# Optimization experiments

Measured on AMD Instinct MI355X. Metric: run time of the kernel, lower is better.

## Reference

```python
import jax, jax.numpy as jnp
import numpy as np

B, H, N, D, RPE = 2, 8, 4096, 64, 64
LAYERS = 3


def _rms(x):
    # SimpleRMSNorm: x / sqrt(mean(x^2) + eps), no learned scale
    return x / jnp.sqrt(jnp.mean(x * x, axis=-1, keepdims=True) + 1e-8)


def setup_inputs() -> dict:
    key = jax.random.key(0)
    ks = jax.random.split(key, 7)
    s = 1.0 / np.sqrt(RPE)
    return {
        "x": jax.random.normal(ks[0], (B, H, N, D), dtype=jnp.float32),
        "w_in": jax.random.normal(ks[1], (1, RPE), dtype=jnp.float32) * 0.5,
        "b_in": jax.random.normal(ks[2], (RPE,), dtype=jnp.float32) * 0.02,
        "w_hid": jax.random.normal(ks[3], (LAYERS, RPE, RPE), dtype=jnp.float32) * s,
        "b_hid": jax.random.normal(ks[4], (LAYERS, RPE), dtype=jnp.float32) * 0.02,
        "w_out": jax.random.normal(ks[5], (RPE, H * D), dtype=jnp.float32) * s,
        "b_out": jax.random.normal(ks[6], (H * D,), dtype=jnp.float32) * 0.02,
    }


def reference(x, w_in, b_in, w_hid, b_hid, w_out, b_out):
    n = x.shape[-2]
    dt = x.dtype

    def rpe(idx):  # idx: (m, 1) relative-position features
        h = idx @ w_in + b_in  # (m, RPE)
        for i in range(LAYERS):  # non-residual: x = layer(x)
            h = jax.nn.relu(_rms(h)) @ w_hid[i] + b_hid[i]
        h = jax.nn.relu(_rms(h)) @ w_out + b_out  # (m, H*D)
        return h.reshape(-1, H, D).transpose(1, 0, 2)  # (H, m, D)

    zero_idx = jnp.ones((1, 1), dt)
    pos_idx = (1.0 / jnp.arange(2, n + 1, dtype=dt)).reshape(n - 1, 1)
    neg_idx = (-1.0 / jnp.arange(n, 1, -1, dtype=dt)).reshape(n - 1, 1)

    zero_k = rpe(zero_idx)  # (H, 1, D); used for both T[0] slots like the torch code
    a = jnp.concatenate([zero_k, rpe(pos_idx), zero_k, rpe(neg_idx)], axis=1)  # (H, 2n, D)
    # act_type='none' -> identity activation on a

    # Toeplitz matvec as circular conv of length 2n via FFT
    y = jnp.fft.rfft(x, 2 * n, axis=-2)          # (B, H, n+1, D) complex
    v = jnp.fft.rfft(a, 2 * n, axis=-2)[None]    # (1, H, n+1, D) complex
    out = jnp.fft.irfft(v * y, 2 * n, axis=-2)[:, :, :n, :]
    return out.astype(dt)
```

## Files before the change

### kernel.cpp

```cpp
#include <hip/hip_runtime.h>

#define N_SEQ 4096
#define N_FFT 8192
#define LAYERS 3
#define FT 512
#define PIDX(i) ((i) + ((i) >> 5))

template<int M>
__device__ inline void pass16_fwd(float* re, float* im, int tid)
{
    const int Q = M >> 4;
    const int j = tid & (Q - 1);
    const int G = tid / Q;
    const int base = G * M + j;
    const float KR[4] = {1.f, 0.9238795325f, 0.7071067812f, 0.3826834324f};
    const float KI[4] = {0.f, -0.3826834324f, -0.7071067812f, -0.9238795325f};
    float xr[4][4], xi[4][4];
#pragma unroll
    for (int a = 0; a < 4; ++a)
#pragma unroll
        for (int b = 0; b < 4; ++b) {
            int idx = PIDX(base + a * (M >> 2) + b * Q);
            xr[a][b] = re[idx]; xi[a][b] = im[idx];
        }
    float cj, sj;
    __sincosf(-6.283185307179586f / (float)M * (float)j, &sj, &cj);
#pragma unroll
    for (int b = 0; b < 4; ++b) {
        float c1 = cj * KR[b] - sj * KI[b];
        float s1 = cj * KI[b] + sj * KR[b];
        float c2 = c1 * c1 - s1 * s1, s2 = 2.f * c1 * s1;
        float c3 = c2 * c1 - s2 * s1, s3 = c2 * s1 + s2 * c1;
        float ar = xr[0][b] + xr[2][b], ai = xi[0][b] + xi[2][b];
        float br = xr[0][b] - xr[2][b], bi = xi[0][b] - xi[2][b];
        float cr = xr[1][b] + xr[3][b], ci = xi[1][b] + xi[3][b];
        float dr = xi[1][b] - xi[3][b], di = -(xr[1][b] - xr[3][b]);
        xr[0][b] = ar + cr;               xi[0][b] = ai + ci;
        float t1r = br + dr, t1i = bi + di;
        xr[1][b] = t1r * c1 - t1i * s1;   xi[1][b] = t1r * s1 + t1i * c1;
        float t2r = ar - cr, t2i = ai - ci;
        xr[2][b] = t2r * c2 - t2i * s2;   xi[2][b] = t2r * s2 + t2i * c2;
        float t3r = br - dr, t3i = bi - di;
        xr[3][b] = t3r * c3 - t3i * s3;   xi[3][b] = t3r * s3 + t3i * c3;
    }
    {
        float e1c = cj * cj - sj * sj, e1s = 2.f * cj * sj;
        float c1 = e1c * e1c - e1s * e1s, s1 = 2.f * e1c * e1s;
        float c2 = c1 * c1 - s1 * s1, s2 = 2.f * c1 * s1;
        float c3 = c2 * c1 - s2 * s1, s3 = c2 * s1 + s2 * c1;
#pragma unroll
        for (int a = 0; a < 4; ++a) {
            float ar = xr[a][0] + xr[a][2], ai = xi[a][0] + xi[a][2];
            float br = xr[a][0] - xr[a][2], bi = xi[a][0] - xi[a][2];
            float cr = xr[a][1] + xr[a][3], ci = xi[a][1] + xi[a][3];
            float dr = xi[a][1] - xi[a][3], di = -(xr[a][1] - xr[a][3]);
            xr[a][0] = ar + cr;               xi[a][0] = ai + ci;
            float t1r = br + dr, t1i = bi + di;
            xr[a][1] = t1r * c1 - t1i * s1;   xi[a][1] = t1r * s1 + t1i * c1;
            float t2r = ar - cr, t2i = ai - ci;
            xr[a][2] = t2r * c2 - t2i * s2;   xi[a][2] = t2r * s2 + t2i * c2;
            float t3r = br - dr, t3i = bi - di;
            xr[a][3] = t3r * c3 - t3i * s3;   xi[a][3] = t3r * s3 + t3i * c3;
        }
    }
#pragma unroll
    for (int a = 0; a < 4; ++a)
#pragma unroll
        for (int b = 0; b < 4; ++b) {
            int idx = PIDX(base + a * (M >> 2) + b * Q);
            re[idx] = xr[a][b]; im[idx] = xi[a][b];
        }
}

template<int M>
__device__ inline void pass16_inv(float* re, float* im, int tid)
{
    const int Q = M >> 4;
    const int j = tid & (Q - 1);
    const int G = tid / Q;
    const int base = G * M + j;
    const float KR[4] = {1.f, 0.9238795325f, 0.7071067812f, 0.3826834324f};
    const float KI[4] = {0.f, 0.3826834324f, 0.7071067812f, 0.9238795325f};
    float xr[4][4], xi[4][4];
#pragma unroll
    for (int a = 0; a < 4; ++a)
#pragma unroll
        for (int b = 0; b < 4; ++b) {
            int idx = PIDX(base + a * (M >> 2) + b * Q);
            xr[a][b] = re[idx]; xi[a][b] = im[idx];
        }
    float cj, sj;
    __sincosf(6.283185307179586f / (float)M * (float)j, &sj, &cj);
    {
        float e1c = cj * cj - sj * sj, e1s = 2.f * cj * sj;
        float c1 = e1c * e1c - e1s * e1s, s1 = 2.f * e1c * e1s;
        float c2 = c1 * c1 - s1 * s1, s2 = 2.f * c1 * s1;
        float c3 = c2 * c1 - s2 * s1, s3 = c2 * s1 + s2 * c1;
#pragma unroll
        for (int a = 0; a < 4; ++a) {
            float t0r = xr[a][0], t0i = xi[a][0];
            float t1r = xr[a][1] * c1 - xi[a][1] * s1, t1i = xr[a][1] * s1 + xi[a][1] * c1;
            float t2r = xr[a][2] * c2 - xi[a][2] * s2, t2i = xr[a][2] * s2 + xi[a][2] * c2;
            float t3r = xr[a][3] * c3 - xi[a][3] * s3, t3i = xr[a][3] * s3 + xi[a][3] * c3;
            float pr = t0r + t2r, pi = t0i + t2i;
            float qr = t0r - t2r, qi = t0i - t2i;
            float rr = t1r + t3r, ri = t1i + t3i;
            float sr = -(t1i - t3i), si = t1r - t3r;
            xr[a][0] = pr + rr; xi[a][0] = pi + ri;
            xr[a][1] = qr + sr; xi[a][1] = qi + si;
            xr[a][2] = pr - rr; xi[a][2] = pi - ri;
            xr[a][3] = qr - sr; xi[a][3] = qi - si;
        }
    }
#pragma unroll
    for (int b = 0; b < 4; ++b) {
        float c1 = cj * KR[b] - sj * KI[b];
        float s1 = cj * KI[b] + sj * KR[b];
        float c2 = c1 * c1 - s1 * s1, s2 = 2.f * c1 * s1;
        float c3 = c2 * c1 - s2 * s1, s3 = c2 * s1 + s2 * c1;
        float t0r = xr[0][b], t0i = xi[0][b];
        float t1r = xr[1][b] * c1 - xi[1][b] * s1, t1i = xr[1][b] * s1 + xi[1][b] * c1;
        float t2r = xr[2][b] * c2 - xi[2][b] * s2, t2i = xr[2][b] * s2 + xi[2][b] * c2;
        float t3r = xr[3][b] * c3 - xi[3][b] * s3, t3i = xr[3][b] * s3 + xi[3][b] * c3;
        float pr = t0r + t2r, pi = t0i + t2i;
        float qr = t0r - t2r, qi = t0i - t2i;
        float rr = t1r + t3r, ri = t1i + t3i;
        float sr = -(t1i - t3i), si = t1r - t3r;
        xr[0][b] = pr + rr; xi[0][b] = pi + ri;
        xr[1][b] = qr + sr; xi[1][b] = qi + si;
        xr[2][b] = pr - rr; xi[2][b] = pi - ri;
        xr[3][b] = qr - sr; xi[3][b] = qi - si;
    }
#pragma unroll
    for (int a = 0; a < 4; ++a)
#pragma unroll
        for (int b = 0; b < 4; ++b) {
            int idx = PIDX(base + a * (M >> 2) + b * Q);
            re[idx] = xr[a][b]; im[idx] = xi[a][b];
        }
}

__device__ inline void fwd8(float* zr, float* zi, int o)
{
    const float R = 0.70710678118654752f;
    {
        float ar = zr[o] + zr[o+4], ai = zi[o] + zi[o+4];
        float br = zr[o] - zr[o+4], bi = zi[o] - zi[o+4];
        float cr = zr[o+2] + zr[o+6], ci = zi[o+2] + zi[o+6];
        float dr = zi[o+2] - zi[o+6], di = -(zr[o+2] - zr[o+6]);
        zr[o]   = ar + cr; zi[o]   = ai + ci;
        zr[o+2] = br + dr; zi[o+2] = bi + di;
        zr[o+4] = ar - cr; zi[o+4] = ai - ci;
        zr[o+6] = br - dr; zi[o+6] = bi - di;
    }
    {
        float ar = zr[o+1] + zr[o+5], ai = zi[o+1] + zi[o+5];
        float br = zr[o+1] - zr[o+5], bi = zi[o+1] - zi[o+5];
        float cr = zr[o+3] + zr[o+7], ci = zi[o+3] + zi[o+7];
        float dr = zi[o+3] - zi[o+7], di = -(zr[o+3] - zr[o+7]);
        zr[o+1] = ar + cr; zi[o+1] = ai + ci;
        float t1r = br + dr, t1i = bi + di;
        zr[o+3] = R * (t1r + t1i); zi[o+3] = R * (t1i - t1r);
        float t2r = ar - cr, t2i = ai - ci;
        zr[o+5] = t2i;  zi[o+5] = -t2r;
        float t3r = br - dr, t3i = bi - di;
        zr[o+7] = R * (t3i - t3r); zi[o+7] = -R * (t3r + t3i);
    }
#pragma unroll
    for (int p = 0; p < 8; p += 2) {
        float ur = zr[o+p], ui = zi[o+p], vr = zr[o+p+1], vi = zi[o+p+1];
        zr[o+p]   = ur + vr; zi[o+p]   = ui + vi;
        zr[o+p+1] = ur - vr; zi[o+p+1] = ui - vi;
    }
}

__device__ inline void inv8(float* zr, float* zi, int o)
{
    const float R = 0.70710678118654752f;
#pragma unroll
    for (int p = 0; p < 8; p += 2) {
        float ur = zr[o+p], ui = zi[o+p], vr = zr[o+p+1], vi = zi[o+p+1];
        zr[o+p]   = ur + vr; zi[o+p]   = ui + vi;
        zr[o+p+1] = ur - vr; zi[o+p+1] = ui - vi;
    }
    {
        float t0r = zr[o],   t0i = zi[o];
        float t1r = zr[o+2], t1i = zi[o+2];
        float t2r = zr[o+4], t2i = zi[o+4];
        float t3r = zr[o+6], t3i = zi[o+6];
        float pr = t0r + t2r, pi = t0i + t2i;
        float qr = t0r - t2r, qi = t0i - t2i;
        float rr = t1r + t3r, ri = t1i + t3i;
        float sr = -(t1i - t3i), si = t1r - t3r;
        zr[o]   = pr + rr; zi[o]   = pi + ri;
        zr[o+2] = qr + sr; zi[o+2] = qi + si;
        zr[o+4] = pr - rr; zi[o+4] = pi - ri;
        zr[o+6] = qr - sr; zi[o+6] = qi - si;
    }
    {
        float t0r = zr[o+1], t0i = zi[o+1];
        float yr = zr[o+3], yi = zi[o+3];
        float t1r = R * (yr - yi), t1i = R * (yr + yi);
        yr = zr[o+5]; yi = zi[o+5];
        float t2r = -yi, t2i = yr;
        yr = zr[o+7]; yi = zi[o+7];
        float t3r = -R * (yr + yi), t3i = R * (yr - yi);
        float pr = t0r + t2r, pi = t0i + t2i;
        float qr = t0r - t2r, qi = t0i - t2i;
        float rr = t1r + t3r, ri = t1i + t3i;
        float sr = -(t1i - t3i), si = t1r - t3r;
        zr[o+1] = pr + rr; zi[o+1] = pi + ri;
        zr[o+3] = qr + sr; zi[o+3] = qi + si;
        zr[o+5] = pr - rr; zi[o+5] = pi - ri;
        zr[o+7] = qr - sr; zi[o+7] = qi - si;
    }
}

__global__ __launch_bounds__(512, 4) void prep_kernel(
    const float* __restrict__ x,
    const float* __restrict__ w_in, const float* __restrict__ b_in,
    const float* __restrict__ w_hid, const float* __restrict__ b_hid,
    const float* __restrict__ w_out, const float* __restrict__ b_out,
    float* __restrict__ a_t, float2* __restrict__ xt2)
{
    __shared__ __align__(16) char smem[43264];
    const int tid = threadIdx.x;

    if (blockIdx.x >= 256) {
        float (*t0)[65] = (float (*)[65])smem;
        float (*t1)[65] = (float (*)[65])(smem + 16640);
        int bb = blockIdx.x - 256;
        int h = bb >> 6;
        int nb = bb & 63;
        int lx = tid & 63;
        int ly = tid >> 6;
        const float* s0 = x + ((size_t)h * N_SEQ + nb * 64) * 64;
        const float* s1 = x + ((size_t)(8 + h) * N_SEQ + nb * 64) * 64;
        for (int r = ly; r < 64; r += 8) {
            t0[r][lx] = s0[r * 64 + lx];
            t1[r][lx] = s1[r * 64 + lx];
        }
        __syncthreads();
        for (int r = ly; r < 64; r += 8) {
            float2* dst = xt2 + (size_t)(h * 64 + r) * N_SEQ + nb * 64;
            dst[lx] = make_float2(t0[lx][r], t1[lx][r]);
        }
        return;
    }

    float (*ubuf)[65] = (float (*)[65])smem;
    float (*sums)[17] = (float (*)[17])(smem + 8320);
    float4* wl        = (float4*)(smem + 10496);

    {
        const int p = tid & 31;
        const int s = tid >> 5;
        const int pos = blockIdx.x * 32 + p;
        float v;
        if (pos == 0 || pos == N_SEQ) v = 1.0f;
        else if (pos < N_SEQ)         v = 1.0f / (float)(pos + 1);
        else                          v = -1.0f / (float)(2 * N_SEQ + 1 - pos);

        float h[4];
#pragma unroll
        for (int i = 0; i < 4; ++i) {
            int f = s * 4 + i;
            h[i] = v * w_in[f] + b_in[f];
        }
        for (int L = 0; L < LAYERS; ++L) {
            const float4* wsrc = (const float4*)(w_hid + L * 4096);
            wl[tid] = wsrc[tid];
            wl[tid + 512] = wsrc[tid + 512];
            float s2 = h[0]*h[0] + h[1]*h[1] + h[2]*h[2] + h[3]*h[3];
            sums[p][s] = s2;
            __syncthreads();
            float tot = 0.f;
#pragma unroll
            for (int g = 0; g < 16; ++g) tot += sums[p][g];
            float r = rsqrtf(tot * (1.f / 64.f) + 1e-8f);
#pragma unroll
            for (int i = 0; i < 4; ++i)
                ubuf[p][s * 4 + i] = fmaxf(h[i] * r, 0.f);
            __syncthreads();
            float acc[4];
#pragma unroll
            for (int i = 0; i < 4; ++i) acc[i] = b_hid[L * 64 + s * 4 + i];
#pragma unroll 8
            for (int j = 0; j < 64; ++j) {
                float uj = ubuf[p][j];
                float4 w = wl[j * 16 + s];
                acc[0] = fmaf(uj, w.x, acc[0]); acc[1] = fmaf(uj, w.y, acc[1]);
                acc[2] = fmaf(uj, w.z, acc[2]); acc[3] = fmaf(uj, w.w, acc[3]);
            }
#pragma unroll
            for (int i = 0; i < 4; ++i) h[i] = acc[i];
            __syncthreads();
        }
        float s2 = h[0]*h[0] + h[1]*h[1] + h[2]*h[2] + h[3]*h[3];
        sums[p][s] = s2;
        __syncthreads();
        float tot = 0.f;
#pragma unroll
        for (int g = 0; g < 16; ++g) tot += sums[p][g];
        float r = rsqrtf(tot * (1.f / 64.f) + 1e-8f);
#pragma unroll
        for (int i = 0; i < 4; ++i)
            ubuf[p][s * 4 + i] = fmaxf(h[i] * r, 0.f);
        __syncthreads();
    }

    {
        const int o  = tid >> 3;
        const int pg = tid & 7;
        const int pos0 = blockIdx.x * 32;
        float4* wt = wl;
        float acc[8][4];
#pragma unroll
        for (int ii = 0; ii < 8; ++ii) {
            float bo = b_out[o * 8 + ii];
#pragma unroll
            for (int i = 0; i < 4; ++i) acc[ii][i] = bo;
        }
        for (int jc = 0; jc < 4; ++jc) {
            float4 wreg[4];
#pragma unroll
            for (int k = 0; k < 4; ++k) {
                int i4 = k * 512 + tid;
                int jj = i4 >> 7, f4 = i4 & 127;
                wreg[k] = *(const float4*)(w_out + (jc * 16 + jj) * 512 + f4 * 4);
            }
            __syncthreads();
#pragma unroll
            for (int k = 0; k < 4; ++k) {
                int i4 = k * 512 + tid;
                wt[i4] = wreg[k];
            }
            __syncthreads();
#pragma unroll
            for (int jj = 0; jj < 16; ++jj) {
                int j = jc * 16 + jj;
                float4 w0 = wt[jj * 128 + o * 2];
                float4 w1 = wt[jj * 128 + o * 2 + 1];
                float u0 = ubuf[pg * 4 + 0][j];
                float u1 = ubuf[pg * 4 + 1][j];
                float u2 = ubuf[pg * 4 + 2][j];
                float u3 = ubuf[pg * 4 + 3][j];
                acc[0][0] = fmaf(u0, w0.x, acc[0][0]); acc[0][1] = fmaf(u1, w0.x, acc[0][1]);
                acc[0][2] = fmaf(u2, w0.x, acc[0][2]); acc[0][3] = fmaf(u3, w0.x, acc[0][3]);
                acc[1][0] = fmaf(u0, w0.y, acc[1][0]); acc[1][1] = fmaf(u1, w0.y, acc[1][1]);
                acc[1][2] = fmaf(u2, w0.y, acc[1][2]); acc[1][3] = fmaf(u3, w0.y, acc[1][3]);
                acc[2][0] = fmaf(u0, w0.z, acc[2][0]); acc[2][1] = fmaf(u1, w0.z, acc[2][1]);
                acc[2][2] = fmaf(u2, w0.z, acc[2][2]); acc[2][3] = fmaf(u3, w0.z, acc[2][3]);
                acc[3][0] = fmaf(u0, w0.w, acc[3][0]); acc[3][1] = fmaf(u1, w0.w, acc[3][1]);
                acc[3][2] = fmaf(u2, w0.w, acc[3][2]); acc[3][3] = fmaf(u3, w0.w, acc[3][3]);
                acc[4][0] = fmaf(u0, w1.x, acc[4][0]); acc[4][1] = fmaf(u1, w1.x, acc[4][1]);
                acc[4][2] = fmaf(u2, w1.x, acc[4][2]); acc[4][3] = fmaf(u3, w1.x, acc[4][3]);
                acc[5][0] = fmaf(u0, w1.y, acc[5][0]); acc[5][1] = fmaf(u1, w1.y, acc[5][1]);
                acc[5][2] = fmaf(u2, w1.y, acc[5][2]); acc[5][3] = fmaf(u3, w1.y, acc[5][3]);
                acc[6][0] = fmaf(u0, w1.z, acc[6][0]); acc[6][1] = fmaf(u1, w1.z, acc[6][1]);
                acc[6][2] = fmaf(u2, w1.z, acc[6][2]); acc[6][3] = fmaf(u3, w1.z, acc[6][3]);
                acc[7][0] = fmaf(u0, w1.w, acc[7][0]); acc[7][1] = fmaf(u1, w1.w, acc[7][1]);
                acc[7][2] = fmaf(u2, w1.w, acc[7][2]); acc[7][3] = fmaf(u3, w1.w, acc[7][3]);
            }
            __syncthreads();
        }
#pragma unroll
        for (int ii = 0; ii < 8; ++ii) {
            int f = o * 8 + ii;
#pragma unroll
            for (int i = 0; i < 4; ++i)
                a_t[(size_t)f * N_FFT + pos0 + pg * 4 + i] = acc[ii][i];
        }
    }
}

__global__ __launch_bounds__(FT, 2) void conv_kernel(const float* __restrict__ a_t,
                                                     const float2* __restrict__ xt2,
                                                     float2* __restrict__ out_t2)
{
    __shared__ float re[8448];
    __shared__ float im[8448];
    const int tid = threadIdx.x;
    const int hd = blockIdx.x;
    const float JR = 0.9238795325f;
    const float JI = -0.3826834324f;

    {
        const float* src = a_t + (size_t)hd * N_FFT;
        float ck, sk;
        __sincosf(-6.283185307179586f / 8192.f * (float)tid, &sk, &ck);
#pragma unroll
        for (int pp = 0; pp < 4; ++pp) {
            int k = pp * FT + tid;
            float x0 = src[k], x1 = src[k + 2048], x2 = src[k + 4096], x3 = src[k + 6144];
            float ar = x0 + x2, br = x0 - x2;
            float cr = x1 + x3, e = x1 - x3;
            re[PIDX(k)] = ar + cr; im[PIDX(k)] = 0.f;
            float c1 = ck, s1 = sk;
            float c2 = c1 * c1 - s1 * s1, s2 = 2.f * c1 * s1;
            float c3 = c2 * c1 - s2 * s1, s3 = c2 * s1 + s2 * c1;
            re[PIDX(k + 2048)] = br * c1 + e * s1;  im[PIDX(k + 2048)] = br * s1 - e * c1;
            float t2r = ar - cr;
            re[PIDX(k + 4096)] = t2r * c2;          im[PIDX(k + 4096)] = t2r * s2;
            re[PIDX(k + 6144)] = br * c3 - e * s3;  im[PIDX(k + 6144)] = br * s3 + e * c3;
            float tc = ck * JR - sk * JI; sk = ck * JI + sk * JR; ck = tc;
        }
    }
    __syncthreads();
    pass16_fwd<2048>(re, im, tid);
    __syncthreads();
    pass16_fwd<128>(re, im, tid);
    __syncthreads();
    float afr[16], afi[16];
    {
        const int base = tid * 16;
#pragma unroll
        for (int c = 0; c < 16; ++c) { int idx = PIDX(base + c); afr[c] = re[idx]; afi[c] = im[idx]; }
        fwd8(afr, afi, 0); fwd8(afr, afi, 8);
    }
    __syncthreads();
    {
        const float2* src = xt2 + (size_t)hd * N_SEQ;
        float ck, sk;
        __sincosf(-6.283185307179586f / 8192.f * (float)tid, &sk, &ck);
#pragma unroll
        for (int pp = 0; pp < 4; ++pp) {
            int k = pp * FT + tid;
            float2 z0 = src[k], z1 = src[k + 2048];
            float ar = z0.x, ai = z0.y;
            float cr = z1.x, ci = z1.y;
            float dr = z1.y, di = -z1.x;
            re[PIDX(k)] = ar + cr; im[PIDX(k)] = ai + ci;
            float c1 = ck, s1 = sk;
            float c2 = c1 * c1 - s1 * s1, s2 = 2.f * c1 * s1;
            float c3 = c2 * c1 - s2 * s1, s3 = c2 * s1 + s2 * c1;
            float t1r = ar + dr, t1i = ai + di;
            re[PIDX(k + 2048)] = t1r * c1 - t1i * s1; im[PIDX(k + 2048)] = t1r * s1 + t1i * c1;
            float t2r = ar - cr, t2i = ai - ci;
            re[PIDX(k + 4096)] = t2r * c2 - t2i * s2; im[PIDX(k + 4096)] = t2r * s2 + t2i * c2;
            float t3r = ar - dr, t3i = ai - di;
            re[PIDX(k + 6144)] = t3r * c3 - t3i * s3; im[PIDX(k + 6144)] = t3r * s3 + t3i * c3;
            float tc = ck * JR - sk * JI; sk = ck * JI + sk * JR; ck = tc;
        }
    }
    __syncthreads();
    pass16_fwd<2048>(re, im, tid);
    __syncthreads();
    pass16_fwd<128>(re, im, tid);
    __syncthreads();
    {
        const int base = tid * 16;
        float zr[16], zi[16];
#pragma unroll
        for (int c = 0; c < 16; ++c) { int idx = PIDX(base + c); zr[c] = re[idx]; zi[c] = im[idx]; }
        fwd8(zr, zi, 0); fwd8(zr, zi, 8);
        const float inv = 1.0f / (float)N_FFT;
#pragma unroll
        for (int c = 0; c < 16; ++c) {
            float xr = zr[c], xi_ = zi[c];
            zr[c] = (xr * afr[c] - xi_ * afi[c]) * inv;
            zi[c] = (xr * afi[c] + xi_ * afr[c]) * inv;
        }
        inv8(zr, zi, 0); inv8(zr, zi, 8);
#pragma unroll
        for (int c = 0; c < 16; ++c) { int idx = PIDX(base + c); re[idx] = zr[c]; im[idx] = zi[c]; }
    }
    __syncthreads();
    pass16_inv<128>(re, im, tid);
    __syncthreads();
    pass16_inv<2048>(re, im, tid);
    __syncthreads();
    {
        float2* dst = out_t2 + (size_t)hd * N_SEQ;
        float ck, sk;
        __sincosf(6.283185307179586f / 8192.f * (float)tid, &sk, &ck);
        const float JcR = 0.9238795325f, JcI = 0.3826834324f;
#pragma unroll
        for (int pp = 0; pp < 4; ++pp) {
            int k = pp * FT + tid;
            float c1 = ck, s1 = sk;
            float c2 = c1 * c1 - s1 * s1, s2 = 2.f * c1 * s1;
            float c3 = c2 * c1 - s2 * s1, s3 = c2 * s1 + s2 * c1;
            float t0r = re[PIDX(k)],        t0i = im[PIDX(k)];
            float y1r = re[PIDX(k + 2048)], y1i = im[PIDX(k + 2048)];
            float y2r = re[PIDX(k + 4096)], y2i = im[PIDX(k + 4096)];
            float y3r = re[PIDX(k + 6144)], y3i = im[PIDX(k + 6144)];
            float t1r = y1r * c1 - y1i * s1, t1i = y1r * s1 + y1i * c1;
            float t2r = y2r * c2 - y2i * s2, t2i = y2r * s2 + y2i * c2;
            float t3r = y3r * c3 - y3i * s3, t3i = y3r * s3 + y3i * c3;
            float pr = t0r + t2r, pi = t0i + t2i;
            float qr = t0r - t2r, qi = t0i - t2i;
            float rr = t1r + t3r, ri = t1i + t3i;
            float sr = -(t1i - t3i), si = t1r - t3r;
            dst[k]        = make_float2(pr + rr, pi + ri);
            dst[k + 2048] = make_float2(qr + sr, qi + si);
            float tc = ck * JcR - sk * JcI; sk = ck * JcI + sk * JcR; ck = tc;
        }
    }
}

__global__ __launch_bounds__(256) void transpose_o_kernel(const float2* __restrict__ out_t2,
                                                          float* __restrict__ out)
{
    __shared__ float t0[64][65];
    __shared__ float t1[64][65];
    int h = blockIdx.x >> 6;
    int nb = blockIdx.x & 63;
    int lx = threadIdx.x & 63;
    int ly = threadIdx.x >> 6;
    for (int r = ly; r < 64; r += 4) {
        float2 v = out_t2[(size_t)(h * 64 + r) * N_SEQ + nb * 64 + lx];
        t0[r][lx] = v.x;
        t1[r][lx] = v.y;
    }
    __syncthreads();
    float* d0 = out + ((size_t)h * N_SEQ + nb * 64) * 64;
    float* d1 = out + ((size_t)(8 + h) * N_SEQ + nb * 64) * 64;
    for (int r = ly; r < 64; r += 4) {
        d0[r * 64 + lx] = t0[lx][r];
        d1[r * 64 + lx] = t1[lx][r];
    }
}

extern "C" void kernel_launch(void* const* d_in, const int* in_sizes, int n_in,
                              void* d_out, int out_size, void* d_ws, size_t ws_size,
                              hipStream_t stream)
{
    const float* x     = (const float*)d_in[0];
    const float* w_in  = (const float*)d_in[1];
    const float* b_in  = (const float*)d_in[2];
    const float* w_hid = (const float*)d_in[3];
    const float* b_hid = (const float*)d_in[4];
    const float* w_out = (const float*)d_in[5];
    const float* b_out = (const float*)d_in[6];
    float* out = (float*)d_out;

    char* ws = (char*)d_ws;
    float2* xt2    = (float2*)ws;
    float*  a_t    = (float*)(ws + (size_t)16 * 1024 * 1024);
    float2* out_t2 = (float2*)(ws + (size_t)32 * 1024 * 1024);

    prep_kernel<<<768, 512, 0, stream>>>(x, w_in, b_in, w_hid, b_hid, w_out, b_out,
                                         a_t, xt2);
    conv_kernel<<<512, FT, 0, stream>>>(a_t, xt2, out_t2);
    transpose_o_kernel<<<512, 256, 0, stream>>>(out_t2, out);
}
```

Before: 143.3 us.

## Restructure FFT conv as radix-8 head plus per-wave 1024-point sub-FFTs

Reworks the 8192-point FFT convolution kernel. A radix-8 first stage now runs in registers on global loads and stores, and the remaining 1024-point sub-transforms are each owned by a single wavefront. This lets the middle passes use wave-level barriers instead of block-wide __syncthreads. Shared memory moves from split re/im arrays to interleaved float2 with vectorized float4 accesses and new padding, and occupancy is raised to 4 blocks. The aim is to cut barrier overhead and LDS traffic. The cost is a more complex index layout, plus higher shared-memory use per block that may limit the requested occupancy.

```diff
diff --git a/kernel.cpp b/kernel.cpp
--- a/kernel.cpp
+++ b/kernel.cpp
@@ -4,15 +4,140 @@
 #define N_FFT 8192
 #define LAYERS 3
 #define FT 512
-#define PIDX(i) ((i) + ((i) >> 5))
+
+#define IDX2(i) ((i) + (((i) >> 5) << 1))
+
+#define WSYNC() { asm volatile("s_waitcnt lgkmcnt(0)" ::: "memory"); __builtin_amdgcn_wave_barrier(); }
+
+__device__ __forceinline__ float2 cmulf(float2 a, float2 b) {
+    return make_float2(fmaf(a.x, b.x, -a.y * b.y), fmaf(a.x, b.y, a.y * b.x));
+}
+__device__ __forceinline__ float2 cmulcf(float2 a, float2 b) {
+    return make_float2(fmaf(a.x, b.x, a.y * b.y), fmaf(a.y, b.x, -a.x * b.y));
+}
+__device__ __forceinline__ float2 f2a(float2 a, float2 b) { return make_float2(a.x + b.x, a.y + b.y); }
+__device__ __forceinline__ float2 f2s(float2 a, float2 b) { return make_float2(a.x - b.x, a.y - b.y); }
+
+__device__ __forceinline__ void twchain(int np, float2* T)
+{
+    float c1, s1;
+    __sincosf(-7.6699039394282061e-4f * (float)np, &s1, &c1);
+    T[1] = make_float2(c1, s1);
+    T[2] = cmulf(T[1], T[1]);
+    T[3] = cmulf(T[2], T[1]);
+    T[4] = cmulf(T[2], T[2]);
+    T[5] = cmulf(T[3], T[2]);
+    T[6] = cmulf(T[3], T[3]);
+    T[7] = cmulf(T[4], T[3]);
+}
+
+__device__ __forceinline__ void ahead8(const float* x, int np, float2* X)
+{
+    const float R2 = 0.70710678118654752f;
+    float p0 = x[0] + x[4], q0 = x[0] - x[4];
+    float p1 = x[2] + x[6], q1 = x[2] - x[6];
+    float r0 = x[1] + x[5], t0 = x[1] - x[5];
+    float r1 = x[3] + x[7], t1 = x[3] - x[7];
+    float e0 = p0 + p1, e2 = p0 - p1;
+    float o0 = r0 + r1, o2 = r0 - r1;
+    float rm = R2 * (t0 - t1), rp = R2 * (t0 + t1);
+    X[0] = make_float2(e0 + o0, 0.f);
+    X[4] = make_float2(e0 - o0, 0.f);
+    X[2] = make_float2(e2, -o2);
+    X[6] = make_float2(e2,  o2);
+    X[1] = make_float2(q0 + rm, -q1 - rp);
+    X[5] = make_float2(q0 - rm, -q1 + rp);
+    X[3] = make_float2(q0 - rm,  q1 - rp);
+    X[7] = make_float2(q0 + rm,  q1 + rp);
+    float2 T[8];
+    twchain(np, T);
+#pragma unroll
+    for (int q = 1; q < 8; ++q) X[q] = cmulf(X[q], T[q]);
+}
+
+__device__ __forceinline__ void zhead8(const float2* z, int np, float2* X)
+{
+    const float R2 = 0.70710678118654752f;
+    float2 A0 = f2a(z[0], z[2]);
+    float2 A2 = f2s(z[0], z[2]);
+    float2 A1 = make_float2(z[0].x + z[2].y, z[0].y - z[2].x);
+    float2 A3 = make_float2(z[0].x - z[2].y, z[0].y + z[2].x);
+    float2 B0 = f2a(z[1], z[3]);
+    float2 bm = f2s(z[1], z[3]);
+    float2 B2 = make_float2(bm.y, -bm.x);
+    float2 u1 = make_float2(z[1].x + z[3].y, z[1].y - z[3].x);
+    float2 B1 = make_float2(R2 * (u1.x + u1.y), R2 * (u1.y - u1.x));
+    float2 u3 = make_float2(z[1].x - z[3].y, z[1].y + z[3].x);
+    float2 B3 = make_float2(R2 * (u3.y - u3.x), -R2 * (u3.x + u3.y));
+    X[0] = f2a(A0, B0); X[4] = f2s(A0, B0);
+    X[1] = f2a(A1, B1); X[5] = f2s(A1, B1);
+    X[2] = f2a(A2, B2); X[6] = f2s(A2, B2);
+    X[3] = f2a(A3, B3); X[7] = f2s(A3, B3);
+    float2 T[8];
+    twchain(np, T);
+#pragma unroll
+    for (int q = 1; q < 8; ++q) X[q] = cmulf(X[q], T[q]);
+}
+
+__device__ __forceinline__ void ihead8(const float2* v, int np, float2* u)
+{
+    const float R2 = 0.70710678118654752f;
+    float2 T[8];
+    twchain(np, T);
+    float2 V[8];
+    V[0] = v[0];
+#pragma unroll
+    for (int q = 1; q < 8; ++q) V[q] = cmulcf(v[q], T[q]);
+    float2 s0 = f2a(V[0], V[4]), d0 = f2s(V[0], V[4]);
+    float2 s1 = f2a(V[1], V[5]), d1 = f2s(V[1], V[5]);
+    float2 s2 = f2a(V[2], V[6]), d2 = f2s(V[2], V[6]);
+    float2 s3 = f2a(V[3], V[7]), d3 = f2s(V[3], V[7]);
+    u[0] = f2a(f2a(s0, s1), f2a(s2, s3));
+    u[2] = make_float2((s0.x - s2.x) - (s1.y - s3.y),
+                       (s0.y - s2.y) + (s1.x - s3.x));
+    float m1 = R2 * (d1.x - d1.y), p1 = R2 * (d1.x + d1.y);
+    float m3 = R2 * (d3.x - d3.y), p3 = R2 * (d3.x + d3.y);
+    u[1] = make_float2(d0.x + m1 - d2.y - p3, d0.y + p1 + d2.x + m3);
+    u[3] = make_float2(d0.x - p1 + d2.y + m3, d0.y + m1 - d2.x + p3);
+}
+
+__device__ __forceinline__ void tail4_fwd(float2* y)
+{
+#pragma unroll
+    for (int g = 0; g < 16; g += 4) {
+        float2 a = f2a(y[g],     y[g + 2]);
+        float2 b = f2s(y[g],     y[g + 2]);
+        float2 c = f2a(y[g + 1], y[g + 3]);
+        float2 w = f2s(y[g + 1], y[g + 3]);
+        float2 d = make_float2(w.y, -w.x);
+        y[g]     = f2a(a, c);
+        y[g + 1] = f2a(b, d);
+        y[g + 2] = f2s(a, c);
+        y[g + 3] = f2s(b, d);
+    }
+}
+__device__ __forceinline__ void tail4_inv(float2* y)
+{
+#pragma unroll
+    for (int g = 0; g < 16; g += 4) {
+        float2 a = f2a(y[g],     y[g + 2]);
+        float2 b = f2s(y[g],     y[g + 2]);
+        float2 c = f2a(y[g + 1], y[g + 3]);
+        float2 d = f2s(y[g + 1], y[g + 3]);
+        float2 id = make_float2(-d.y, d.x);
+        y[g]     = f2a(a, c);
+        y[g + 2] = f2s(a, c);
+        y[g + 1] = f2a(b, id);
+        y[g + 3] = f2s(b, id);
+    }
+}
 
 template<int M>
-__device__ inline void pass16_fwd(float* re, float* im, int tid)
+__device__ __forceinline__ void wpass16_fwd(float2* buf, int C, int lane)
 {
     const int Q = M >> 4;
-    const int j = tid & (Q - 1);
-    const int G = tid / Q;
-    const int base = G * M + j;
+    const int j = lane & (Q - 1);
+    const int base = C + (lane / Q) * M + j;
     const float KR[4] = {1.f, 0.9238795325f, 0.7071067812f, 0.3826834324f};
     const float KI[4] = {0.f, -0.3826834324f, -0.7071067812f, -0.9238795325f};
     float xr[4][4], xi[4][4];
@@ -20,8 +145,8 @@
     for (int a = 0; a < 4; ++a)
 #pragma unroll
         for (int b = 0; b < 4; ++b) {
-            int idx = PIDX(base + a * (M >> 2) + b * Q);
-            xr[a][b] = re[idx]; xi[a][b] = im[idx];
+            float2 v = buf[IDX2(base + a * (M >> 2) + b * Q)];
+            xr[a][b] = v.x; xi[a][b] = v.y;
         }
     float cj, sj;
     __sincosf(-6.283185307179586f / (float)M * (float)j, &sj, &cj);
@@ -66,19 +191,16 @@
 #pragma unroll
     for (int a = 0; a < 4; ++a)
 #pragma unroll
-        for (int b = 0; b < 4; ++b) {
-            int idx = PIDX(base + a * (M >> 2) + b * Q);
-            re[idx] = xr[a][b]; im[idx] = xi[a][b];
-        }
+        for (int b = 0; b < 4; ++b)
+            buf[IDX2(base + a * (M >> 2) + b * Q)] = make_float2(xr[a][b], xi[a][b]);
 }
 
 template<int M>
-__device__ inline void pass16_inv(float* re, float* im, int tid)
+__device__ __forceinline__ void wpass16_inv(float2* buf, int C, int lane)
 {
     const int Q = M >> 4;
-    const int j = tid & (Q - 1);
-    const int G = tid / Q;
-    const int base = G * M + j;
+    const int j = lane & (Q - 1);
+    const int base = C + (lane / Q) * M + j;
     const float KR[4] = {1.f, 0.9238795325f, 0.7071067812f, 0.3826834324f};
     const float KI[4] = {0.f, 0.3826834324f, 0.7071067812f, 0.9238795325f};
     float xr[4][4], xi[4][4];
@@ -86,8 +208,8 @@
     for (int a = 0; a < 4; ++a)
 #pragma unroll
         for (int b = 0; b < 4; ++b) {
-            int idx = PIDX(base + a * (M >> 2) + b * Q);
-            xr[a][b] = re[idx]; xi[a][b] = im[idx];
+            float2 v = buf[IDX2(base + a * (M >> 2) + b * Q)];
+            xr[a][b] = v.x; xi[a][b] = v.y;
         }
     float cj, sj;
     __sincosf(6.283185307179586f / (float)M * (float)j, &sj, &cj);
@@ -134,86 +256,8 @@
 #pragma unroll
     for (int a = 0; a < 4; ++a)
 #pragma unroll
-        for (int b = 0; b < 4; ++b) {
-            int idx = PIDX(base + a * (M >> 2) + b * Q);
-            re[idx] = xr[a][b]; im[idx] = xi[a][b];
-        }
-}
-
-__device__ inline void fwd8(float* zr, float* zi, int o)
-{
-    const float R = 0.70710678118654752f;
-    {
-        float ar = zr[o] + zr[o+4], ai = zi[o] + zi[o+4];
-        float br = zr[o] - zr[o+4], bi = zi[o] - zi[o+4];
-        float cr = zr[o+2] + zr[o+6], ci = zi[o+2] + zi[o+6];
-        float dr = zi[o+2] - zi[o+6], di = -(zr[o+2] - zr[o+6]);
-        zr[o]   = ar + cr; zi[o]   = ai + ci;
-        zr[o+2] = br + dr; zi[o+2] = bi + di;
-        zr[o+4] = ar - cr; zi[o+4] = ai - ci;
-        zr[o+6] = br - dr; zi[o+6] = bi - di;
-    }
-    {
-        float ar = zr[o+1] + zr[o+5], ai = zi[o+1] + zi[o+5];
-        float br = zr[o+1] - zr[o+5], bi = zi[o+1] - zi[o+5];
-        float cr = zr[o+3] + zr[o+7], ci = zi[o+3] + zi[o+7];
-        float dr = zi[o+3] - zi[o+7], di = -(zr[o+3] - zr[o+7]);
-        zr[o+1] = ar + cr; zi[o+1] = ai + ci;
-        float t1r = br + dr, t1i = bi + di;
-        zr[o+3] = R * (t1r + t1i); zi[o+3] = R * (t1i - t1r);
-        float t2r = ar - cr, t2i = ai - ci;
-        zr[o+5] = t2i;  zi[o+5] = -t2r;
-        float t3r = br - dr, t3i = bi - di;
-        zr[o+7] = R * (t3i - t3r); zi[o+7] = -R * (t3r + t3i);
-    }
-#pragma unroll
-    for (int p = 0; p < 8; p += 2) {
-        float ur = zr[o+p], ui = zi[o+p], vr = zr[o+p+1], vi = zi[o+p+1];
-        zr[o+p]   = ur + vr; zi[o+p]   = ui + vi;
-        zr[o+p+1] = ur - vr; zi[o+p+1] = ui - vi;
-    }
-}
-
-__device__ inline void inv8(float* zr, float* zi, int o)
-{
-    const float R = 0.70710678118654752f;
-#pragma unroll
-    for (int p = 0; p < 8; p += 2) {
-        float ur = zr[o+p], ui = zi[o+p], vr = zr[o+p+1], vi = zi[o+p+1];
-        zr[o+p]   = ur + vr; zi[o+p]   = ui + vi;
-        zr[o+p+1] = ur - vr; zi[o+p+1] = ui - vi;
-    }
-    {
-        float t0r = zr[o],   t0i = zi[o];
-        float t1r = zr[o+2], t1i = zi[o+2];
-        float t2r = zr[o+4], t2i = zi[o+4];
-        float t3r = zr[o+6], t3i = zi[o+6];
-        float pr = t0r + t2r, pi = t0i + t2i;
-        float qr = t0r - t2r, qi = t0i - t2i;
-        float rr = t1r + t3r, ri = t1i + t3i;
-        float sr = -(t1i - t3i), si = t1r - t3r;
-        zr[o]   = pr + rr; zi[o]   = pi + ri;
-        zr[o+2] = qr + sr; zi[o+2] = qi + si;
-        zr[o+4] = pr - rr; zi[o+4] = pi - ri;
-        zr[o+6] = qr - sr; zi[o+6] = qi - si;
-    }
-    {
-        float t0r = zr[o+1], t0i = zi[o+1];
-        float yr = zr[o+3], yi = zi[o+3];
-        float t1r = R * (yr - yi), t1i = R * (yr + yi);
-        yr = zr[o+5]; yi = zi[o+5];
-        float t2r = -yi, t2i = yr;
-        yr = zr[o+7]; yi = zi[o+7];
-        float t3r = -R * (yr + yi), t3i = R * (yr - yi);
-        float pr = t0r + t2r, pi = t0i + t2i;
-        float qr = t0r - t2r, qi = t0i - t2i;
-        float rr = t1r + t3r, ri = t1i + t3i;
-        float sr = -(t1i - t3i), si = t1r - t3r;
-        zr[o+1] = pr + rr; zi[o+1] = pi + ri;
-        zr[o+3] = qr + sr; zi[o+3] = qi + si;
-        zr[o+5] = pr - rr; zi[o+5] = pi - ri;
-        zr[o+7] = qr - sr; zi[o+7] = qi - si;
-    }
+        for (int b = 0; b < 4; ++b)
+            buf[IDX2(base + a * (M >> 2) + b * Q)] = make_float2(xr[a][b], xi[a][b]);
 }
 
 __global__ __launch_bounds__(512, 4) void prep_kernel(
@@ -374,128 +418,113 @@
     }
 }
 
-__global__ __launch_bounds__(FT, 2) void conv_kernel(const float* __restrict__ a_t,
+__global__ __launch_bounds__(FT, 4) void conv_kernel(const float* __restrict__ a_t,
                                                      const float2* __restrict__ xt2,
                                                      float2* __restrict__ out_t2)
 {
-    __shared__ float re[8448];
-    __shared__ float im[8448];
+    __shared__ __align__(16) float2 buf[8704];
     const int tid = threadIdx.x;
+    const int lane = tid & 63;
+    const int C = (tid >> 6) << 10;
     const int hd = blockIdx.x;
-    const float JR = 0.9238795325f;
-    const float JI = -0.3826834324f;
-
-    {
-        const float* src = a_t + (size_t)hd * N_FFT;
-        float ck, sk;
-        __sincosf(-6.283185307179586f / 8192.f * (float)tid, &sk, &ck);
-#pragma unroll
-        for (int pp = 0; pp < 4; ++pp) {
-            int k = pp * FT + tid;
-            float x0 = src[k], x1 = src[k + 2048], x2 = src[k + 4096], x3 = src[k + 6144];
-            float ar = x0 + x2, br = x0 - x2;
-            float cr = x1 + x3, e = x1 - x3;
-            re[PIDX(k)] = ar + cr; im[PIDX(k)] = 0.f;
-            float c1 = ck, s1 = sk;
-            float c2 = c1 * c1 - s1 * s1, s2 = 2.f * c1 * s1;
-            float c3 = c2 * c1 - s2 * s1, s3 = c2 * s1 + s2 * c1;
-            re[PIDX(k + 2048)] = br * c1 + e * s1;  im[PIDX(k + 2048)] = br * s1 - e * c1;
-            float t2r = ar - cr;
-            re[PIDX(k + 4096)] = t2r * c2;          im[PIDX(k + 4096)] = t2r * s2;
-            re[PIDX(k + 6144)] = br * c3 - e * s3;  im[PIDX(k + 6144)] = br * s3 + e * c3;
-            float tc = ck * JR - sk * JI; sk = ck * JI + sk * JR; ck = tc;
-        }
+
+    {
+        const float2* asrc = (const float2*)(a_t + (size_t)hd * N_FFT);
+        float2 av[8];
+#pragma unroll
+        for (int p = 0; p < 8; ++p) av[p] = asrc[tid + 512 * p];
+        float xa[8], xb[8];
+#pragma unroll
+        for (int p = 0; p < 8; ++p) { xa[p] = av[p].x; xb[p] = av[p].y; }
+        float2 X0[8], X1[8];
+        ahead8(xa, 2 * tid,     X0);
+        ahead8(xb, 2 * tid + 1, X1);
+#pragma unroll
+        for (int q = 0; q < 8; ++q)
+            *(float4*)&buf[IDX2(q * 1024 + 2 * tid)] =
+                make_float4(X0[q].x, X0[q].y, X1[q].x, X1[q].y);
     }
     __syncthreads();
-    pass16_fwd<2048>(re, im, tid);
+    wpass16_fwd<1024>(buf, C, lane);
+    WSYNC();
+    wpass16_fwd<64>(buf, C, lane);
+    WSYNC();
+    float2 asp[16];
+#pragma unroll
+    for (int k = 0; k < 8; ++k) {
+        float4 v = *(const float4*)&buf[IDX2(C + 16 * lane + 2 * k)];
+        asp[2 * k]     = make_float2(v.x, v.y);
+        asp[2 * k + 1] = make_float2(v.z, v.w);
+    }
+    tail4_fwd(asp);
+    float4 zl[4];
+    {
+        const float4* zsrc = (const float4*)(xt2 + (size_t)hd * N_SEQ);
+#pragma unroll
+        for (int p = 0; p < 4; ++p) zl[p] = zsrc[tid + 512 * p];
+    }
     __syncthreads();
-    pass16_fwd<128>(re, im, tid);
+    {
+        float2 z0[4], z1[4];
+#pragma unroll
+        for (int p = 0; p < 4; ++p) {
+            z0[p] = make_float2(zl[p].x, zl[p].y);
+            z1[p] = make_float2(zl[p].z, zl[p].w);
+        }
+        float2 X0[8], X1[8];
+        zhead8(z0, 2 * tid,     X0);
+        zhead8(z1, 2 * tid + 1, X1);
+#pragma unroll
+        for (int q = 0; q < 8; ++q)
+            *(float4*)&buf[IDX2(q * 1024 + 2 * tid)] =
+                make_float4(X0[q].x, X0[q].y, X1[q].x, X1[q].y);
+    }
     __syncthreads();
-    float afr[16], afi[16];
-    {
-        const int base = tid * 16;
-#pragma unroll
-        for (int c = 0; c < 16; ++c) { int idx = PIDX(base + c); afr[c] = re[idx]; afi[c] = im[idx]; }
-        fwd8(afr, afi, 0); fwd8(afr, afi, 8);
-    }
+    wpass16_fwd<1024>(buf, C, lane);
+    WSYNC();
+    wpass16_fwd<64>(buf, C, lane);
+    WSYNC();
+    {
+        float2 zp[16];
+#pragma unroll
+        for (int k = 0; k < 8; ++k) {
+            float4 v = *(const float4*)&buf[IDX2(C + 16 * lane + 2 * k)];
+            zp[2 * k]     = make_float2(v.x, v.y);
+            zp[2 * k + 1] = make_float2(v.z, v.w);
+        }
+        tail4_fwd(zp);
+        const float inv = 1.0f / (float)N_FFT;
+#pragma unroll
+        for (int c = 0; c < 16; ++c) {
+            float2 m = cmulf(zp[c], asp[c]);
+            zp[c] = make_float2(m.x * inv, m.y * inv);
+        }
+        tail4_inv(zp);
+#pragma unroll
+        for (int k = 0; k < 8; ++k)
+            *(float4*)&buf[IDX2(C + 16 * lane + 2 * k)] =
+                make_float4(zp[2 * k].x, zp[2 * k].y, zp[2 * k + 1].x, zp[2 * k + 1].y);
+    }
+    WSYNC();
+    wpass16_inv<64>(buf, C, lane);
+    WSYNC();
+    wpass16_inv<1024>(buf, C, lane);
     __syncthreads();
     {
-        const float2* src = xt2 + (size_t)hd * N_SEQ;
-        float ck, sk;
-        __sincosf(-6.283185307179586f / 8192.f * (float)tid, &sk, &ck);
-#pragma unroll
-        for (int pp = 0; pp < 4; ++pp) {
-            int k = pp * FT + tid;
-            float2 z0 = src[k], z1 = src[k + 2048];
-            float ar = z0.x, ai = z0.y;
-            float cr = z1.x, ci = z1.y;
-            float dr = z1.y, di = -z1.x;
-            re[PIDX(k)] = ar + cr; im[PIDX(k)] = ai + ci;
-            float c1 = ck, s1 = sk;
-            float c2 = c1 * c1 - s1 * s1, s2 = 2.f * c1 * s1;
-            float c3 = c2 * c1 - s2 * s1, s3 = c2 * s1 + s2 * c1;
-            float t1r = ar + dr, t1i = ai + di;
-            re[PIDX(k + 2048)] = t1r * c1 - t1i * s1; im[PIDX(k + 2048)] = t1r * s1 + t1i * c1;
-            float t2r = ar - cr, t2i = ai - ci;
-            re[PIDX(k + 4096)] = t2r * c2 - t2i * s2; im[PIDX(k + 4096)] = t2r * s2 + t2i * c2;
-            float t3r = ar - dr, t3i = ai - di;
-            re[PIDX(k + 6144)] = t3r * c3 - t3i * s3; im[PIDX(k + 6144)] = t3r * s3 + t3i * c3;
-            float tc = ck * JR - sk * JI; sk = ck * JI + sk * JR; ck = tc;
-        }
-    }
-    __syncthreads();
-    pass16_fwd<2048>(re, im, tid);
-    __syncthreads();
-    pass16_fwd<128>(re, im, tid);
-    __syncthreads();
-    {
-        const int base = tid * 16;
-        float zr[16], zi[16];
-#pragma unroll
-        for (int c = 0; c < 16; ++c) { int idx = PIDX(base + c); zr[c] = re[idx]; zi[c] = im[idx]; }
-        fwd8(zr, zi, 0); fwd8(zr, zi, 8);
-        const float inv = 1.0f / (float)N_FFT;
-#pragma unroll
-        for (int c = 0; c < 16; ++c) {
-            float xr = zr[c], xi_ = zi[c];
-            zr[c] = (xr * afr[c] - xi_ * afi[c]) * inv;
-            zi[c] = (xr * afi[c] + xi_ * afr[c]) * inv;
-        }
-        inv8(zr, zi, 0); inv8(zr, zi, 8);
-#pragma unroll
-        for (int c = 0; c < 16; ++c) { int idx = PIDX(base + c); re[idx] = zr[c]; im[idx] = zi[c]; }
-    }
-    __syncthreads();
-    pass16_inv<128>(re, im, tid);
-    __syncthreads();
-    pass16_inv<2048>(re, im, tid);
-    __syncthreads();
-    {
-        float2* dst = out_t2 + (size_t)hd * N_SEQ;
-        float ck, sk;
-        __sincosf(6.283185307179586f / 8192.f * (float)tid, &sk, &ck);
-        const float JcR = 0.9238795325f, JcI = 0.3826834324f;
-#pragma unroll
-        for (int pp = 0; pp < 4; ++pp) {
-            int k = pp * FT + tid;
-            float c1 = ck, s1 = sk;
-            float c2 = c1 * c1 - s1 * s1, s2 = 2.f * c1 * s1;
-            float c3 = c2 * c1 - s2 * s1, s3 = c2 * s1 + s2 * c1;
-            float t0r = re[PIDX(k)],        t0i = im[PIDX(k)];
-            float y1r = re[PIDX(k + 2048)], y1i = im[PIDX(k + 2048)];
-            float y2r = re[PIDX(k + 4096)], y2i = im[PIDX(k + 4096)];
-            float y3r = re[PIDX(k + 6144)], y3i = im[PIDX(k + 6144)];
-            float t1r = y1r * c1 - y1i * s1, t1i = y1r * s1 + y1i * c1;
-            float t2r = y2r * c2 - y2i * s2, t2i = y2r * s2 + y2i * c2;
-            float t3r = y3r * c3 - y3i * s3, t3i = y3r * s3 + y3i * c3;
-            float pr = t0r + t2r, pi = t0i + t2i;
-            float qr = t0r - t2r, qi = t0i - t2i;
-            float rr = t1r + t3r, ri = t1i + t3i;
-            float sr = -(t1i - t3i), si = t1r - t3r;
-            dst[k]        = make_float2(pr + rr, pi + ri);
-            dst[k + 2048] = make_float2(qr + sr, qi + si);
-            float tc = ck * JcR - sk * JcI; sk = ck * JcI + sk * JcR; ck = tc;
-        }
+        float2 v0[8], v1[8];
+#pragma unroll
+        for (int q = 0; q < 8; ++q) {
+            float4 r = *(const float4*)&buf[IDX2(q * 1024 + 2 * tid)];
+            v0[q] = make_float2(r.x, r.y);
+            v1[q] = make_float2(r.z, r.w);
+        }
+        float2 u0[4], u1[4];
+        ihead8(v0, 2 * tid,     u0);
+        ihead8(v1, 2 * tid + 1, u1);
+        float4* dst = (float4*)(out_t2 + (size_t)hd * N_SEQ);
+#pragma unroll
+        for (int p = 0; p < 4; ++p)
+            dst[tid + 512 * p] = make_float4(u0[p].x, u0[p].y, u1[p].x, u1[p].y);
     }
 }
 
```

After: 210.9 us. 1.47x slower.
